# Kernel optimization log

Hardware: AMD Instinct MI355X
Metric: run time of the kernel (lower is better)

Reference implementation:

```python
import jax, jax.numpy as jnp
import numpy as np

N = 50000   # nodes
D = 128     # input_dim
E = 1600000 # edges
K = 100     # out_nodes


def setup_inputs() -> dict:
    key = jax.random.key(0)
    ks = jax.random.split(key, 9)
    x = jax.random.normal(ks[0], (N, D), dtype=jnp.float32)
    edge_index = jax.random.randint(ks[1], (2, E), 0, N, dtype=jnp.int64)
    # PyG GCNConv params: Linear(in,out,bias=False) weight + separate bias
    s = 1.0 / np.sqrt(D)
    W1 = jax.random.uniform(ks[2], (D, D), jnp.float32, -s, s)
    b1 = jnp.zeros((D,), jnp.float32)
    W2 = jax.random.uniform(ks[3], (D, D), jnp.float32, -s, s)
    b2 = jnp.zeros((D,), jnp.float32)
    Wa = jax.random.uniform(ks[4], (D, K), jnp.float32, -s, s)
    ba = jax.random.uniform(ks[5], (K,), jnp.float32, -s, s)
    return {"x": x, "edge_index": edge_index, "W1": W1, "b1": b1,
            "W2": W2, "b2": b2, "Wa": Wa, "ba": ba}


def _gcn_conv(x, src, dst, norm, W, b, n_nodes):
    # PyG GCNConv: h = x @ W; aggregate D^-1/2 (A+I) D^-1/2 h; add bias
    h = x @ W                                  # [N, D]
    msg = h[src] * norm[:, None]               # [E+N, D] gather + scale
    agg = jax.ops.segment_sum(msg, dst, num_segments=n_nodes)  # scatter-add
    return agg + b


def reference(x, edge_index, W1, b1, W2, b2, Wa, ba):
    n = x.shape[0]
    loop = jnp.arange(n, dtype=edge_index.dtype)
    src = jnp.concatenate([edge_index[0], loop])   # add self-loops
    dst = jnp.concatenate([edge_index[1], loop])
    deg = jnp.zeros((n,), x.dtype).at[dst].add(1.0)
    dinv = jnp.where(deg > 0, jax.lax.rsqrt(deg), 0.0)
    norm = dinv[src] * dinv[dst]                   # [E+N]

    h = _gcn_conv(x, src, dst, norm, W1, b1, n)
    h = jax.nn.relu(h)
    h = _gcn_conv(h, src, dst, norm, W2, b2, n)
    s = jax.nn.softmax(h @ Wa + ba, axis=1)        # [N, K]
    return s
```

## Files before the change

kernel.cpp:

```cpp
#include <hip/hip_runtime.h>

#define D 128
#define KOUT 100
#define CHUNK 4096

typedef __attribute__((ext_vector_type(8))) short short8;
typedef __attribute__((ext_vector_type(4))) float floatx4;

__device__ inline float bf_lo(unsigned int u) { return __uint_as_float(u << 16); }
__device__ inline float bf_hi(unsigned int u) { return __uint_as_float(u & 0xFFFF0000u); }

__device__ inline unsigned int bf_round(float a) {
    unsigned int ua = __float_as_uint(a);
    return (ua + 0x7FFFu + ((ua >> 16) & 1u)) >> 16;
}
__device__ inline unsigned int pack_bf(float a, float b) {
    return bf_round(a) | (bf_round(b) << 16);
}


__launch_bounds__(256)
__global__ void bucket_pass1(const int* __restrict__ ei, int E, int nbuck, int cap,
                             int* __restrict__ bcur, unsigned int* __restrict__ bdata) {
    __shared__ int hist[256];
    __shared__ int sc[256];
    __shared__ int pfx[256];
    __shared__ int cur[256];
    __shared__ int gbase[256];
    __shared__ unsigned int lbuf[CHUNK];
    __shared__ unsigned char bkt[CHUNK];

    int tid = threadIdx.x;
    int base = blockIdx.x * CHUNK;
    int cnt = E - base; if (cnt > CHUNK) cnt = CHUNK;

    hist[tid] = 0;
    __syncthreads();

    int src[CHUNK / 256];
    int dst[CHUNK / 256];
#pragma unroll
    for (int q = 0; q < CHUNK / 256; q++) {
        int li = tid + q * 256;
        if (li < cnt) {
            src[q] = ei[base + li];
            dst[q] = ei[E + base + li];
            atomicAdd(&hist[dst[q] >> 8], 1);
        }
    }
    __syncthreads();

    int v = hist[tid];
    sc[tid] = v;
    __syncthreads();
    for (int off = 1; off < 256; off <<= 1) {
        int t = (tid >= off) ? sc[tid - off] : 0;
        __syncthreads();
        sc[tid] += t;
        __syncthreads();
    }
    int excl = sc[tid] - v;
    pfx[tid] = excl;
    cur[tid] = excl;
    gbase[tid] = 0;
    if (tid < nbuck && v > 0) gbase[tid] = atomicAdd(&bcur[tid], v);
    __syncthreads();

#pragma unroll
    for (int q = 0; q < CHUNK / 256; q++) {
        int li = tid + q * 256;
        if (li < cnt) {
            int b = dst[q] >> 8;
            int p = atomicAdd(&cur[b], 1);
            lbuf[p] = (unsigned int)src[q] | ((unsigned int)(dst[q] & 255) << 24);
            bkt[p] = (unsigned char)b;
        }
    }
    __syncthreads();

    for (int p = tid; p < cnt; p += 256) {
        int b = bkt[p];
        bdata[(size_t)b * cap + gbase[b] + (p - pfx[b])] = lbuf[p];
    }
}


__launch_bounds__(256)
__global__ void bucket_build(const unsigned int* __restrict__ bdata, const int* __restrict__ bcur,
                             int cap, float* __restrict__ dinv,
                             int* __restrict__ rowptr, int* __restrict__ csr, int n, int nbuck) {
    __shared__ int cnts[256];
    __shared__ int sc[256];
    __shared__ int cur[256];
    __shared__ int bbase;

    int b = blockIdx.x, tid = threadIdx.x;
    if (tid == 0) bbase = 0;
    cnts[tid] = 0;
    __syncthreads();

    int part = 0;
    for (int t = tid; t < b; t += 256) part += bcur[t];
#pragma unroll
    for (int off = 32; off > 0; off >>= 1) part += __shfl_down(part, off);
    if ((tid & 63) == 0 && part != 0) atomicAdd(&bbase, part);

    int cnt = bcur[b];
    const unsigned int* p = bdata + (size_t)b * cap;
    for (int e = tid; e < cnt; e += 256) atomicAdd(&cnts[p[e] >> 24], 1);
    __syncthreads();

    int v = cnts[tid];
    sc[tid] = v;
    __syncthreads();
    for (int off = 1; off < 256; off <<= 1) {
        int t = (tid >= off) ? sc[tid - off] : 0;
        __syncthreads();
        sc[tid] += t;
        __syncthreads();
    }
    int gstart = bbase + (sc[tid] - v);
    int node = b * 256 + tid;
    if (node < n) {
        dinv[node] = rsqrtf((float)(v + 1));
        rowptr[node] = gstart;
    }
    cur[tid] = gstart;
    __syncthreads();

    for (int e = tid; e < cnt; e += 256) {
        unsigned int u = p[e];
        int pos = atomicAdd(&cur[u >> 24], 1);
        csr[pos] = (int)(u & 0xFFFFFFu);
    }
}


__global__ void prep_frag_kernel(const float* __restrict__ W1, const float* __restrict__ W2,
                                 const float* __restrict__ Wa, const float* __restrict__ ba,
                                 const float* __restrict__ b2,
                                 unsigned short* __restrict__ Wf1, unsigned short* __restrict__ WfF,
                                 float* __restrict__ bpad,
                                 int* __restrict__ bcur, int* __restrict__ rowptr,
                                 unsigned int* __restrict__ zrowA, unsigned int* __restrict__ zrowB,
                                 int n, int E) {
    int idx = blockIdx.x * blockDim.x + threadIdx.x;
    if (idx < 2 * 16384) {
        int m = idx >> 14;
        int e = idx & 16383;
        int j = e & 7, lane = (e >> 3) & 63, ct = (e >> 9) & 7, kt = e >> 12;
        int k = kt * 32 + (lane >> 4) * 8 + j;
        int col = ct * 16 + (lane & 15);
        if (m == 0) {
            Wf1[e] = (unsigned short)bf_round(W1[k * 128 + col]);
        } else {
            float s = 0.f;
            if (col < KOUT) {
                const float* w2r = W2 + k * 128;
#pragma unroll 8
                for (int mm = 0; mm < 128; mm++)
                    s = fmaf(w2r[mm], Wa[mm * KOUT + col], s);
            }
            WfF[e] = (unsigned short)bf_round(s);
        }
    }
    if (idx < 128) {
        float s = 0.f;
        if (idx < KOUT) {
            for (int mm = 0; mm < 128; mm++)
                s = fmaf(b2[mm], Wa[mm * KOUT + idx], s);
            s += ba[idx];
        }
        bpad[idx] = s;
    }
    if (idx < 256) bcur[idx] = 0;
    if (idx < 64) { zrowA[idx] = 0u; zrowB[idx] = 0u; }
    if (idx == 256) rowptr[n] = E;
}


__launch_bounds__(256)
__global__ void gemm_mfma_kernel(const void* __restrict__ Xin, const unsigned short* __restrict__ Wf,
                                 const float* __restrict__ bias, const float* __restrict__ oscale,
                                 void* __restrict__ Y, int nrows, int in_bf16, int out_mode) {
    __shared__ float lds_f[64 * 130];
    unsigned short* lds_h = (unsigned short*)lds_f;
    unsigned int* lds_u = (unsigned int*)lds_f;

    int tid = threadIdx.x;
    int w = tid >> 6, lane = tid & 63;
    int quad = lane >> 4, m16 = lane & 15;
    int r0 = blockIdx.x * 64;

    if (!in_bf16) {
        int row = tid >> 2, cg_ = tid & 3;
        bool valid = (r0 + row) < nrows;
        const float4* Xr = (const float4*)Xin + (size_t)(r0 + row) * 32 + cg_ * 8;
#pragma unroll
        for (int j = 0; j < 8; j++) {
            float4 v = valid ? Xr[j] : make_float4(0.f, 0.f, 0.f, 0.f);
            int c = cg_ * 32 + j * 4;
            lds_u[row * 68 + (c >> 1)]     = pack_bf(v.x, v.y);
            lds_u[row * 68 + (c >> 1) + 1] = pack_bf(v.z, v.w);
        }
        __syncthreads();
    }

    floatx4 acc[8];
#pragma unroll
    for (int ct = 0; ct < 8; ct++) acc[ct] = (floatx4){0.f, 0.f, 0.f, 0.f};

    int arow = r0 + w * 16 + m16;
    if (arow > nrows - 1) arow = nrows - 1;
    const unsigned int* Xb = (const unsigned int*)Xin;

    const short8* Wf8 = (const short8*)Wf;
#pragma unroll
    for (int kt = 0; kt < 4; kt++) {
        short8 a;
        if (in_bf16) {
            a = *(const short8*)(Xb + (size_t)arow * 64 + kt * 16 + quad * 4);
        } else {
            a = *(const short8*)(lds_h + (w * 16 + m16) * 136 + kt * 32 + quad * 8);
        }
#pragma unroll
        for (int ct = 0; ct < 8; ct++) {
            short8 b = Wf8[(kt * 8 + ct) * 64 + lane];
            acc[ct] = __builtin_amdgcn_mfma_f32_16x16x32_bf16(a, b, acc[ct], 0, 0, 0);
        }
    }

    if (out_mode == 1) {
        __syncthreads();
#pragma unroll
        for (int ct = 0; ct < 8; ct++) {
#pragma unroll
            for (int r = 0; r < 4; r++) {
                int rl = w * 16 + quad * 4 + r;
                lds_f[rl * 130 + ct * 16 + m16] = acc[ct][r];
            }
        }
        __syncthreads();
        unsigned int* Yb = (unsigned int*)Y;
        for (int r = 0; r < 16; r++) {
            int row = r0 + w * 16 + r;
            if (row < nrows) {
                float sc = oscale ? oscale[row] : 1.f;
                float lo = lds_f[(w * 16 + r) * 130 + 2 * lane] * sc;
                float hi = lds_f[(w * 16 + r) * 130 + 2 * lane + 1] * sc;
                Yb[(size_t)row * 64 + lane] = pack_bf(lo, hi);
            }
        }
    } else {
        float bb[8];
#pragma unroll
        for (int ct = 0; ct < 8; ct++) bb[ct] = bias[ct * 16 + m16];
        float* Yf = (float*)Y;
#pragma unroll
        for (int r = 0; r < 4; r++) {
            int row = r0 + w * 16 + quad * 4 + r;
            float vv[8];
            float mx = -1e30f;
#pragma unroll
            for (int ct = 0; ct < 8; ct++) {
                int col = ct * 16 + m16;
                vv[ct] = (col < KOUT) ? acc[ct][r] + bb[ct] : -1e30f;
                mx = fmaxf(mx, vv[ct]);
            }
#pragma unroll
            for (int off = 1; off < 16; off <<= 1) mx = fmaxf(mx, __shfl_xor(mx, off));
            float se = 0.f;
#pragma unroll
            for (int ct = 0; ct < 8; ct++) {
                vv[ct] = (vv[ct] > -1e29f) ? __expf(vv[ct] - mx) : 0.f;
                se += vv[ct];
            }
#pragma unroll
            for (int off = 1; off < 16; off <<= 1) se += __shfl_xor(se, off);
            float inv = 1.f / se;
            if (row < nrows) {
#pragma unroll
                for (int ct = 0; ct < 8; ct++) {
                    int col = ct * 16 + m16;
                    if (col < KOUT) Yf[(size_t)row * KOUT + col] = vv[ct] * inv;
                }
            }
        }
    }
}


__launch_bounds__(256)
__global__ void aggregate_kernel(const uint4* __restrict__ Hb4, const int* __restrict__ csr,
                                 const int* __restrict__ rowptr,
                                 const float* __restrict__ dinv, const float* __restrict__ bias,
                                 unsigned int* __restrict__ Ob, int n, int do_relu, int post_scale) {
    int wid = threadIdx.x >> 6, lane = threadIdx.x & 63;
    int g = lane >> 4, c = lane & 15;
    int i = blockIdx.x * 4 + wid;
    if (i >= n) return;

    float di = dinv[i];
    int start = rowptr[i];
    int cnt = rowptr[i + 1] - start;
    const int* cp = csr + start;

    float acc[8];
    {
        uint4 sv = Hb4[(size_t)i * 16 + c];
        unsigned int su[4] = {sv.x, sv.y, sv.z, sv.w};
        if (g != 0) { su[0] = su[1] = su[2] = su[3] = 0u; }
#pragma unroll
        for (int t = 0; t < 4; t++) {
            acc[2 * t]     = bf_lo(su[t]);
            acc[2 * t + 1] = bf_hi(su[t]);
        }
    }

    int s[4];
#pragma unroll
    for (int u = 0; u < 4; u++) {
        int idx = u * 4 + g;
        s[u] = (idx < cnt) ? cp[idx] : n;
    }
    for (int e = 0; e < cnt; e += 16) {
        uint4 v[4];
#pragma unroll
        for (int u = 0; u < 4; u++) v[u] = Hb4[(size_t)s[u] * 16 + c];
        int ns[4];
#pragma unroll
        for (int u = 0; u < 4; u++) {
            int idx = e + 16 + u * 4 + g;
            ns[u] = (idx < cnt) ? cp[idx] : n;
        }
#pragma unroll
        for (int u = 0; u < 4; u++) {
            unsigned int uu[4] = {v[u].x, v[u].y, v[u].z, v[u].w};
#pragma unroll
            for (int t = 0; t < 4; t++) {
                acc[2 * t]     += bf_lo(uu[t]);
                acc[2 * t + 1] += bf_hi(uu[t]);
            }
        }
#pragma unroll
        for (int u = 0; u < 4; u++) s[u] = ns[u];
    }

#pragma unroll
    for (int j = 0; j < 8; j++) {
        acc[j] += __shfl_xor(acc[j], 16);
        acc[j] += __shfl_xor(acc[j], 32);
    }

    float2 bb = bias ? ((const float2*)bias)[c * 4 + g] : make_float2(0.f, 0.f);
    float fx = acc[g * 2]     * di + bb.x;
    float fy = acc[g * 2 + 1] * di + bb.y;
    if (do_relu) { fx = fmaxf(fx, 0.f); fy = fmaxf(fy, 0.f); }
    if (post_scale) { fx *= di; fy *= di; }
    Ob[(size_t)i * 64 + c * 4 + g] = pack_bf(fx, fy);
}


extern "C" void kernel_launch(void* const* d_in, const int* in_sizes, int n_in,
                              void* d_out, int out_size, void* d_ws, size_t ws_size,
                              hipStream_t stream) {
    const float* x  = (const float*)d_in[0];
    const int*   ei = (const int*)d_in[1];
    const float* W1 = (const float*)d_in[2];
    const float* b1 = (const float*)d_in[3];
    const float* W2 = (const float*)d_in[4];
    const float* b2 = (const float*)d_in[5];
    const float* Wa = (const float*)d_in[6];
    const float* ba = (const float*)d_in[7];
    float* out = (float*)d_out;

    int N = in_sizes[0] / D;
    int E = in_sizes[1] / 2;

    int nbuck = (N + 255) >> 8;
    int cap = ((E / nbuck) + 2048 + 63) & ~63;

    char* w = (char*)d_ws;
    size_t off = 0;
    auto carve = [&](size_t bytes) -> void* {
        void* p = w + off;
        off = (off + bytes + 255) & ~(size_t)255;
        return p;
    };
    float* dinv   = (float*)carve((size_t)N * 4);
    int*   rowptr = (int*)carve((size_t)(N + 1) * 4);
    int*   bcur   = (int*)carve(256 * 4);
    unsigned int* bdata = (unsigned int*)carve((size_t)nbuck * cap * 4);
    int*   csr    = (int*)carve((size_t)E * 4);
    unsigned short* Wf1 = (unsigned short*)carve(16384 * 2);
    unsigned short* WfF = (unsigned short*)carve(16384 * 2);
    float* bpad   = (float*)carve(512);
    unsigned int* HbA = (unsigned int*)carve((size_t)(N + 1) * 64 * 4);
    unsigned int* HbB = (unsigned int*)carve((size_t)(N + 1) * 64 * 4);
    (void)ws_size; (void)n_in; (void)out_size;

    int nbNode4 = (N + 3) / 4;
    int nbGemm = (N + 63) / 64;
    int nbP1 = (E + CHUNK - 1) / CHUNK;

    prep_frag_kernel<<<128, 256, 0, stream>>>(W1, W2, Wa, ba, b2, Wf1, WfF, bpad,
                                              bcur, rowptr,
                                              HbA + (size_t)N * 64, HbB + (size_t)N * 64, N, E);
    bucket_pass1<<<nbP1, 256, 0, stream>>>(ei, E, nbuck, cap, bcur, bdata);
    bucket_build<<<nbuck, 256, 0, stream>>>(bdata, bcur, cap, dinv, rowptr, csr, N, nbuck);

    gemm_mfma_kernel<<<nbGemm, 256, 0, stream>>>(x, Wf1, nullptr, dinv, HbA, N, 0, 1);
    aggregate_kernel<<<nbNode4, 256, 0, stream>>>((const uint4*)HbA, csr, rowptr, dinv, b1, HbB, N, 1, 1);
    aggregate_kernel<<<nbNode4, 256, 0, stream>>>((const uint4*)HbB, csr, rowptr, dinv, nullptr, HbA, N, 0, 0);
    gemm_mfma_kernel<<<nbGemm, 256, 0, stream>>>(HbA, WfF, bpad, nullptr, out, N, 1, 2);
}
```

Measured before the change: 254.8 us.

## Merge prep with bucketing and CSR build with first GEMM via block-range dispatch

Fuses the weight-prep kernel into the edge-bucketing pass and the CSR build into the first GEMM, using block-index ranges so independent work shares a single launch. This lets the first GEMM run concurrently with the CSR construction. Degrees are now counted with global atomics in the bucketing pass, and dinv is recomputed from degree or row length instead of being stored. The aim is fewer launches and less serialization, at the cost of extra global atomics and LDS-sized blocks for the prep work.

Result: slower. 273.6 us (+7.4%).

```diff
diff --git a/kernel.cpp b/kernel.cpp
--- a/kernel.cpp
+++ b/kernel.cpp
@@ -18,179 +18,17 @@
     return bf_round(a) | (bf_round(b) << 16);
 }
 
-
-__launch_bounds__(256)
-__global__ void bucket_pass1(const int* __restrict__ ei, int E, int nbuck, int cap,
-                             int* __restrict__ bcur, unsigned int* __restrict__ bdata) {
-    __shared__ int hist[256];
-    __shared__ int sc[256];
-    __shared__ int pfx[256];
-    __shared__ int cur[256];
-    __shared__ int gbase[256];
-    __shared__ unsigned int lbuf[CHUNK];
-    __shared__ unsigned char bkt[CHUNK];
-
-    int tid = threadIdx.x;
-    int base = blockIdx.x * CHUNK;
-    int cnt = E - base; if (cnt > CHUNK) cnt = CHUNK;
-
-    hist[tid] = 0;
-    __syncthreads();
-
-    int src[CHUNK / 256];
-    int dst[CHUNK / 256];
-#pragma unroll
-    for (int q = 0; q < CHUNK / 256; q++) {
-        int li = tid + q * 256;
-        if (li < cnt) {
-            src[q] = ei[base + li];
-            dst[q] = ei[E + base + li];
-            atomicAdd(&hist[dst[q] >> 8], 1);
-        }
-    }
-    __syncthreads();
-
-    int v = hist[tid];
-    sc[tid] = v;
-    __syncthreads();
-    for (int off = 1; off < 256; off <<= 1) {
-        int t = (tid >= off) ? sc[tid - off] : 0;
-        __syncthreads();
-        sc[tid] += t;
-        __syncthreads();
-    }
-    int excl = sc[tid] - v;
-    pfx[tid] = excl;
-    cur[tid] = excl;
-    gbase[tid] = 0;
-    if (tid < nbuck && v > 0) gbase[tid] = atomicAdd(&bcur[tid], v);
-    __syncthreads();
-
-#pragma unroll
-    for (int q = 0; q < CHUNK / 256; q++) {
-        int li = tid + q * 256;
-        if (li < cnt) {
-            int b = dst[q] >> 8;
-            int p = atomicAdd(&cur[b], 1);
-            lbuf[p] = (unsigned int)src[q] | ((unsigned int)(dst[q] & 255) << 24);
-            bkt[p] = (unsigned char)b;
-        }
-    }
-    __syncthreads();
-
-    for (int p = tid; p < cnt; p += 256) {
-        int b = bkt[p];
-        bdata[(size_t)b * cap + gbase[b] + (p - pfx[b])] = lbuf[p];
-    }
-}
-
-
-__launch_bounds__(256)
-__global__ void bucket_build(const unsigned int* __restrict__ bdata, const int* __restrict__ bcur,
-                             int cap, float* __restrict__ dinv,
-                             int* __restrict__ rowptr, int* __restrict__ csr, int n, int nbuck) {
-    __shared__ int cnts[256];
-    __shared__ int sc[256];
-    __shared__ int cur[256];
-    __shared__ int bbase;
-
-    int b = blockIdx.x, tid = threadIdx.x;
-    if (tid == 0) bbase = 0;
-    cnts[tid] = 0;
-    __syncthreads();
-
-    int part = 0;
-    for (int t = tid; t < b; t += 256) part += bcur[t];
-#pragma unroll
-    for (int off = 32; off > 0; off >>= 1) part += __shfl_down(part, off);
-    if ((tid & 63) == 0 && part != 0) atomicAdd(&bbase, part);
-
-    int cnt = bcur[b];
-    const unsigned int* p = bdata + (size_t)b * cap;
-    for (int e = tid; e < cnt; e += 256) atomicAdd(&cnts[p[e] >> 24], 1);
-    __syncthreads();
-
-    int v = cnts[tid];
-    sc[tid] = v;
-    __syncthreads();
-    for (int off = 1; off < 256; off <<= 1) {
-        int t = (tid >= off) ? sc[tid - off] : 0;
-        __syncthreads();
-        sc[tid] += t;
-        __syncthreads();
-    }
-    int gstart = bbase + (sc[tid] - v);
-    int node = b * 256 + tid;
-    if (node < n) {
-        dinv[node] = rsqrtf((float)(v + 1));
-        rowptr[node] = gstart;
-    }
-    cur[tid] = gstart;
-    __syncthreads();
-
-    for (int e = tid; e < cnt; e += 256) {
-        unsigned int u = p[e];
-        int pos = atomicAdd(&cur[u >> 24], 1);
-        csr[pos] = (int)(u & 0xFFFFFFu);
-    }
-}
-
-
-__global__ void prep_frag_kernel(const float* __restrict__ W1, const float* __restrict__ W2,
-                                 const float* __restrict__ Wa, const float* __restrict__ ba,
-                                 const float* __restrict__ b2,
-                                 unsigned short* __restrict__ Wf1, unsigned short* __restrict__ WfF,
-                                 float* __restrict__ bpad,
-                                 int* __restrict__ bcur, int* __restrict__ rowptr,
-                                 unsigned int* __restrict__ zrowA, unsigned int* __restrict__ zrowB,
-                                 int n, int E) {
-    int idx = blockIdx.x * blockDim.x + threadIdx.x;
-    if (idx < 2 * 16384) {
-        int m = idx >> 14;
-        int e = idx & 16383;
-        int j = e & 7, lane = (e >> 3) & 63, ct = (e >> 9) & 7, kt = e >> 12;
-        int k = kt * 32 + (lane >> 4) * 8 + j;
-        int col = ct * 16 + (lane & 15);
-        if (m == 0) {
-            Wf1[e] = (unsigned short)bf_round(W1[k * 128 + col]);
-        } else {
-            float s = 0.f;
-            if (col < KOUT) {
-                const float* w2r = W2 + k * 128;
-#pragma unroll 8
-                for (int mm = 0; mm < 128; mm++)
-                    s = fmaf(w2r[mm], Wa[mm * KOUT + col], s);
-            }
-            WfF[e] = (unsigned short)bf_round(s);
-        }
-    }
-    if (idx < 128) {
-        float s = 0.f;
-        if (idx < KOUT) {
-            for (int mm = 0; mm < 128; mm++)
-                s = fmaf(b2[mm], Wa[mm * KOUT + idx], s);
-            s += ba[idx];
-        }
-        bpad[idx] = s;
-    }
-    if (idx < 256) bcur[idx] = 0;
-    if (idx < 64) { zrowA[idx] = 0u; zrowB[idx] = 0u; }
-    if (idx == 256) rowptr[n] = E;
-}
-
-
-__launch_bounds__(256)
-__global__ void gemm_mfma_kernel(const void* __restrict__ Xin, const unsigned short* __restrict__ Wf,
-                                 const float* __restrict__ bias, const float* __restrict__ oscale,
-                                 void* __restrict__ Y, int nrows, int in_bf16, int out_mode) {
-    __shared__ float lds_f[64 * 130];
+__device__ void gemm_body(const void* __restrict__ Xin, const unsigned short* __restrict__ Wf,
+                          const float* __restrict__ bias, const int* __restrict__ deg,
+                          void* __restrict__ Y, int nrows, int in_bf16, int out_mode,
+                          float* lds_f, int tile) {
     unsigned short* lds_h = (unsigned short*)lds_f;
     unsigned int* lds_u = (unsigned int*)lds_f;
 
     int tid = threadIdx.x;
     int w = tid >> 6, lane = tid & 63;
     int quad = lane >> 4, m16 = lane & 15;
-    int r0 = blockIdx.x * 64;
+    int r0 = tile * 64;
 
     if (!in_bf16) {
         int row = tid >> 2, cg_ = tid & 3;
@@ -245,7 +83,7 @@
         for (int r = 0; r < 16; r++) {
             int row = r0 + w * 16 + r;
             if (row < nrows) {
-                float sc = oscale ? oscale[row] : 1.f;
+                float sc = deg ? rsqrtf((float)(deg[row] + 1)) : 1.f;
                 float lo = lds_f[(w * 16 + r) * 130 + 2 * lane] * sc;
                 float hi = lds_f[(w * 16 + r) * 130 + 2 * lane + 1] * sc;
                 Yb[(size_t)row * 64 + lane] = pack_bf(lo, hi);
@@ -291,19 +129,195 @@
 
 
 __launch_bounds__(256)
+__global__ void k_p1_prep(const int* __restrict__ ei, int E, int nbuck, int cap,
+                          int* __restrict__ bcur, unsigned int* __restrict__ bdata,
+                          int* __restrict__ deg,
+                          const float* __restrict__ W1, const float* __restrict__ W2,
+                          const float* __restrict__ Wa, const float* __restrict__ ba,
+                          const float* __restrict__ b2,
+                          unsigned short* __restrict__ Wf1, unsigned short* __restrict__ WfF,
+                          float* __restrict__ bpad, int* __restrict__ rowptr,
+                          unsigned int* __restrict__ zrowA, unsigned int* __restrict__ zrowB,
+                          int n, int nbP1) {
+    __shared__ float lds_f[64 * 130];
+    int tid = threadIdx.x;
+
+    if ((int)blockIdx.x < nbP1) {
+        int* hist = (int*)lds_f;
+        int* sc   = hist + 256;
+        int* pfx  = sc + 256;
+        int* cur  = pfx + 256;
+        int* gbase = cur + 256;
+        unsigned int* lbuf = (unsigned int*)(gbase + 256);
+        unsigned char* bkt = (unsigned char*)(lbuf + CHUNK);
+
+        int base = blockIdx.x * CHUNK;
+        int cnt = E - base; if (cnt > CHUNK) cnt = CHUNK;
+
+        hist[tid] = 0;
+        __syncthreads();
+
+        int src[CHUNK / 256];
+        int dst[CHUNK / 256];
+#pragma unroll
+        for (int q = 0; q < CHUNK / 256; q++) {
+            int li = tid + q * 256;
+            if (li < cnt) {
+                src[q] = ei[base + li];
+                dst[q] = ei[E + base + li];
+                atomicAdd(&hist[dst[q] >> 8], 1);
+            }
+        }
+        __syncthreads();
+
+        int v = hist[tid];
+        sc[tid] = v;
+        __syncthreads();
+        for (int off = 1; off < 256; off <<= 1) {
+            int t = (tid >= off) ? sc[tid - off] : 0;
+            __syncthreads();
+            sc[tid] += t;
+            __syncthreads();
+        }
+        int excl = sc[tid] - v;
+        pfx[tid] = excl;
+        cur[tid] = excl;
+        gbase[tid] = 0;
+        if (tid < nbuck && v > 0) gbase[tid] = atomicAdd(&bcur[tid], v);
+        __syncthreads();
+
+#pragma unroll
+        for (int q = 0; q < CHUNK / 256; q++) {
+            int li = tid + q * 256;
+            if (li < cnt) {
+                int b = dst[q] >> 8;
+                int p = atomicAdd(&cur[b], 1);
+                lbuf[p] = (unsigned int)src[q] | ((unsigned int)(dst[q] & 255) << 24);
+                bkt[p] = (unsigned char)b;
+            }
+        }
+        __syncthreads();
+
+        for (int p = tid; p < cnt; p += 256) {
+            int b = bkt[p];
+            unsigned int rec = lbuf[p];
+            bdata[(size_t)b * cap + gbase[b] + (p - pfx[b])] = rec;
+            atomicAdd(deg + b * 256 + (int)(rec >> 24), 1);
+        }
+    } else {
+        int idx = ((int)blockIdx.x - nbP1) * 256 + tid;
+        if (idx < 2 * 16384) {
+            int m = idx >> 14;
+            int e = idx & 16383;
+            int j = e & 7, lane = (e >> 3) & 63, ct = (e >> 9) & 7, kt = e >> 12;
+            int k = kt * 32 + (lane >> 4) * 8 + j;
+            int col = ct * 16 + (lane & 15);
+            if (m == 0) {
+                Wf1[e] = (unsigned short)bf_round(W1[k * 128 + col]);
+            } else {
+                float s = 0.f;
+                if (col < KOUT) {
+                    const float* w2r = W2 + k * 128;
+#pragma unroll 8
+                    for (int mm = 0; mm < 128; mm++)
+                        s = fmaf(w2r[mm], Wa[mm * KOUT + col], s);
+                }
+                WfF[e] = (unsigned short)bf_round(s);
+            }
+        }
+        if (idx < 128) {
+            float s = 0.f;
+            if (idx < KOUT) {
+                for (int mm = 0; mm < 128; mm++)
+                    s = fmaf(b2[mm], Wa[mm * KOUT + idx], s);
+                s += ba[idx];
+            }
+            bpad[idx] = s;
+        }
+        if (idx < 64) { zrowA[idx] = 0u; zrowB[idx] = 0u; }
+        if (idx == 64) rowptr[n] = E;
+    }
+}
+
+
+__launch_bounds__(256)
+__global__ void k_build_gemm(const unsigned int* __restrict__ bdata, const int* __restrict__ bcur,
+                             int cap, int* __restrict__ rowptr, int* __restrict__ csr,
+                             int n, int nbuck,
+                             const float* __restrict__ X, const unsigned short* __restrict__ Wf1,
+                             const int* __restrict__ deg, unsigned int* __restrict__ HbA) {
+    __shared__ float lds_f[64 * 130];
+    int tid = threadIdx.x;
+
+    if ((int)blockIdx.x < nbuck) {
+        int* cnts = (int*)lds_f;
+        int* sc   = cnts + 256;
+        int* cur  = sc + 256;
+        int* pbb  = cur + 256;
+
+        int b = blockIdx.x;
+        if (tid == 0) pbb[0] = 0;
+        cnts[tid] = 0;
+        __syncthreads();
+
+        int part = 0;
+        for (int t = tid; t < b; t += 256) part += bcur[t];
+#pragma unroll
+        for (int off = 32; off > 0; off >>= 1) part += __shfl_down(part, off);
+        if ((tid & 63) == 0 && part != 0) atomicAdd(&pbb[0], part);
+
+        int cnt = bcur[b];
+        const unsigned int* p = bdata + (size_t)b * cap;
+        for (int e = tid; e < cnt; e += 256) atomicAdd(&cnts[p[e] >> 24], 1);
+        __syncthreads();
+
+        int v = cnts[tid];
+        sc[tid] = v;
+        __syncthreads();
+        for (int off = 1; off < 256; off <<= 1) {
+            int t = (tid >= off) ? sc[tid - off] : 0;
+            __syncthreads();
+            sc[tid] += t;
+            __syncthreads();
+        }
+        int gstart = pbb[0] + (sc[tid] - v);
+        int node = b * 256 + tid;
+        if (node < n) rowptr[node] = gstart;
+        cur[tid] = gstart;
+        __syncthreads();
+
+        for (int e = tid; e < cnt; e += 256) {
+            unsigned int u = p[e];
+            int pos = atomicAdd(&cur[u >> 24], 1);
+            csr[pos] = (int)(u & 0xFFFFFFu);
+        }
+    } else {
+        gemm_body(X, Wf1, nullptr, deg, HbA, n, 0, 1, lds_f, (int)blockIdx.x - nbuck);
+    }
+}
+
+__launch_bounds__(256)
+__global__ void k_gemm_final(const void* __restrict__ Xin, const unsigned short* __restrict__ WfF,
+                             const float* __restrict__ bpad, void* __restrict__ out, int n) {
+    __shared__ float lds_f[64 * 130];
+    gemm_body(Xin, WfF, bpad, nullptr, out, n, 1, 2, lds_f, (int)blockIdx.x);
+}
+
+
+__launch_bounds__(256)
 __global__ void aggregate_kernel(const uint4* __restrict__ Hb4, const int* __restrict__ csr,
                                  const int* __restrict__ rowptr,
-                                 const float* __restrict__ dinv, const float* __restrict__ bias,
+                                 const float* __restrict__ bias,
                                  unsigned int* __restrict__ Ob, int n, int do_relu, int post_scale) {
     int wid = threadIdx.x >> 6, lane = threadIdx.x & 63;
     int g = lane >> 4, c = lane & 15;
     int i = blockIdx.x * 4 + wid;
     if (i >= n) return;
 
-    float di = dinv[i];
     int start = rowptr[i];
     int cnt = rowptr[i + 1] - start;
     const int* cp = csr + start;
+    float di = rsqrtf((float)(cnt + 1));
 
     float acc[8];
     {
@@ -387,9 +401,9 @@
         off = (off + bytes + 255) & ~(size_t)255;
         return p;
     };
-    float* dinv   = (float*)carve((size_t)N * 4);
+    int*   bcur   = (int*)carve(256 * 4);
+    int*   deg    = (int*)carve((size_t)N * 4);
     int*   rowptr = (int*)carve((size_t)(N + 1) * 4);
-    int*   bcur   = (int*)carve(256 * 4);
     unsigned int* bdata = (unsigned int*)carve((size_t)nbuck * cap * 4);
     int*   csr    = (int*)carve((size_t)E * 4);
     unsigned short* Wf1 = (unsigned short*)carve(16384 * 2);
@@ -403,14 +417,15 @@
     int nbGemm = (N + 63) / 64;
     int nbP1 = (E + CHUNK - 1) / CHUNK;
 
-    prep_frag_kernel<<<128, 256, 0, stream>>>(W1, W2, Wa, ba, b2, Wf1, WfF, bpad,
-                                              bcur, rowptr,
-                                              HbA + (size_t)N * 64, HbB + (size_t)N * 64, N, E);
-    bucket_pass1<<<nbP1, 256, 0, stream>>>(ei, E, nbuck, cap, bcur, bdata);
-    bucket_build<<<nbuck, 256, 0, stream>>>(bdata, bcur, cap, dinv, rowptr, csr, N, nbuck);
-
-    gemm_mfma_kernel<<<nbGemm, 256, 0, stream>>>(x, Wf1, nullptr, dinv, HbA, N, 0, 1);
-    aggregate_kernel<<<nbNode4, 256, 0, stream>>>((const uint4*)HbA, csr, rowptr, dinv, b1, HbB, N, 1, 1);
-    aggregate_kernel<<<nbNode4, 256, 0, stream>>>((const uint4*)HbB, csr, rowptr, dinv, nullptr, HbA, N, 0, 0);
-    gemm_mfma_kernel<<<nbGemm, 256, 0, stream>>>(HbA, WfF, bpad, nullptr, out, N, 1, 2);
-}
+    (void)hipMemsetAsync(bcur, 0, 1024 + (size_t)N * 4, stream);
+
+    k_p1_prep<<<nbP1 + 128, 256, 0, stream>>>(ei, E, nbuck, cap, bcur, bdata, deg,
+                                              W1, W2, Wa, ba, b2, Wf1, WfF, bpad, rowptr,
+                                              HbA + (size_t)N * 64, HbB + (size_t)N * 64,
+                                              N, nbP1);
+    k_build_gemm<<<nbuck + nbGemm, 256, 0, stream>>>(bdata, bcur, cap, rowptr, csr, N, nbuck,
+                                                     x, Wf1, deg, HbA);
+    aggregate_kernel<<<nbNode4, 256, 0, stream>>>((const uint4*)HbA, csr, rowptr, b1, HbB, N, 1, 1);
+    aggregate_kernel<<<nbNode4, 256, 0, stream>>>((const uint4*)HbB, csr, rowptr, nullptr, HbA, N, 0, 0);
+    k_gemm_final<<<nbGemm, 256, 0, stream>>>(HbA, WfF, bpad, out, N);
+}
```
